# Performance work log

Hardware: AMD Instinct MI355X
Metric: run time of the kernel (lower is better)

Reference implementation:

```python
import jax, jax.numpy as jnp
import numpy as np

NUM_CHANNELS = 512
B_DIM = 64
C_DIM = 16
N = 512
FEAT = NUM_CHANNELS * 4 * 4  # 8192


def setup_inputs() -> dict:
    key = jax.random.key(0)
    k1, k2 = jax.random.split(key)
    inp = jax.random.normal(k1, (N, NUM_CHANNELS, 4, 4), dtype=jnp.float32)
    T = jax.random.normal(k2, (FEAT, B_DIM * C_DIM), dtype=jnp.float32) * 0.1
    return {"inp": inp, "T": T}


def reference(inp, T):
    x = inp.reshape(-1, FEAT)                      # (N, 8192)
    M = (x @ T).reshape(-1, B_DIM, C_DIM)          # (N, B, C)
    # pairwise L1 distance over C: (N, N, B)
    dist = jnp.sum(jnp.abs(M[:, None, :, :] - M[None, :, :, :]), axis=-1)
    o = jnp.sum(jnp.exp(-dist), axis=1)            # (N, B)
    return jnp.concatenate((x, o), axis=1)         # (N, 8192 + B)
```

## Files before the change

kernel.cpp:

```cpp
#include <hip/hip_runtime.h>

#define NROWS 512
#define FEAT  8192
#define BDIM  64
#define CDIM  16
#define MCOLS 1024
#define OUTC  8256
#define KSPLIT 8
#define KCHUNK (FEAT / KSPLIT)
#define MSIZE  (NROWS * MCOLS)

typedef __bf16 bf16x8 __attribute__((ext_vector_type(8)));
typedef float  floatx4 __attribute__((ext_vector_type(4)));

#define AS1 __attribute__((address_space(1)))
#define AS3 __attribute__((address_space(3)))

static __device__ __forceinline__ void gload16(const void* g, void* l) {
    __builtin_amdgcn_global_load_lds((AS1 void*)(g), (AS3 void*)(l), 16, 0, 0);
}

static __device__ __forceinline__ unsigned short f2bf(float f) {
    unsigned int x = __builtin_bit_cast(unsigned int, f);
    unsigned int r = (x + 0x7FFFu + ((x >> 16) & 1u)) >> 16;
    return (unsigned short)r;
}

__global__ __launch_bounds__(512, 2) void k_prep(const float* __restrict__ x,
                                                 const float* __restrict__ T,
                                                 unsigned short* __restrict__ xb,
                                                 unsigned short* __restrict__ Tt,
                                                 float* __restrict__ out) {
    __shared__ __align__(16) float lds[2][64][65];
    int bid = blockIdx.x, t = threadIdx.x;
#pragma unroll
    for (int u = 0; u < 8; ++u) {
        int gid = bid * 4096 + u * 512 + t;
        float4 v = *(const float4*)(x + (size_t)gid * 4);
        ushort4 uu;
        uu.x = f2bf(v.x); uu.y = f2bf(v.y); uu.z = f2bf(v.z); uu.w = f2bf(v.w);
        *(ushort4*)(xb + (size_t)gid * 4) = uu;
        int row = gid >> 11, col4 = gid & 2047;
        *(float4*)(out + (size_t)row * OUTC + col4 * 4) = v;
    }
    int sub = t >> 8, tt = t & 255;
    for (int u = 0; u < 4; ++u) {
        int tile = bid * 8 + u * 2 + sub;
        int kt = tile & 127, nt = tile >> 7;
        __syncthreads();
        int kk = tt >> 2, q = tt & 3;
#pragma unroll
        for (int p = 0; p < 4; ++p) {
            int c4 = q + p * 4;
            float4 v = *(const float4*)(T + (size_t)(kt * 64 + kk) * MCOLS + nt * 64 + c4 * 4);
            lds[sub][kk][c4 * 4 + 0] = v.x; lds[sub][kk][c4 * 4 + 1] = v.y;
            lds[sub][kk][c4 * 4 + 2] = v.z; lds[sub][kk][c4 * 4 + 3] = v.w;
        }
        __syncthreads();
        int nr = tt >> 2, ck = tt & 3;
        unsigned int wv[8];
#pragma unroll
        for (int j = 0; j < 8; ++j) {
            unsigned int lo = f2bf(lds[sub][ck * 16 + j * 2 + 0][nr]);
            unsigned int hi = f2bf(lds[sub][ck * 16 + j * 2 + 1][nr]);
            wv[j] = lo | (hi << 16);
        }
        uint4* dst = (uint4*)(Tt + (size_t)(nt * 64 + nr) * FEAT + kt * 64 + ck * 16);
        dst[0] = make_uint4(wv[0], wv[1], wv[2], wv[3]);
        dst[1] = make_uint4(wv[4], wv[5], wv[6], wv[7]);
    }
}

__global__ __launch_bounds__(256, 2) void k_gemm(const unsigned short* __restrict__ xb,
                                                 const unsigned short* __restrict__ Tt,
                                                 float* __restrict__ Mp) {
    __shared__ __align__(16) unsigned short ldsA[128 * 64];
    __shared__ __align__(16) unsigned short ldsB[64 * 64];
    int bid = blockIdx.x, t = threadIdx.x;
    int mt = bid & 3, nt = (bid >> 2) & 15, ks = bid >> 6;
    int m0 = mt * 128, n0 = nt * 64, kbase = ks * KCHUNK;
    int w = t >> 6, l = t & 63;

    int c  = (l & 3) ^ ((l >> 3) & 3);
    int lr = l >> 2;
    const unsigned short* gA0 = xb + (size_t)(m0 + w * 32 + lr) * FEAT + kbase + c * 8;
    const unsigned short* gA1 = gA0 + (size_t)16 * FEAT;
    const unsigned short* gB0 = Tt + (size_t)(n0 + w * 16 + lr) * FEAT + kbase + c * 8;
    unsigned short* lA00 = ldsA + (4 * w + 0) * 512;
    unsigned short* lA01 = ldsA + (4 * w + 1) * 512;
    unsigned short* lA10 = ldsA + (4 * w + 2) * 512;
    unsigned short* lA11 = ldsA + (4 * w + 3) * 512;
    unsigned short* lB0  = ldsB + (2 * w + 0) * 512;
    unsigned short* lB1  = ldsB + (2 * w + 1) * 512;

    int wr = w >> 1, wc = w & 1, fm = l & 15, fq = l >> 4;
    int fo = fm * 32 + ((fq ^ ((fm >> 1) & 3)) * 8);
    const unsigned short* paB = ldsA + (wr * 8) * 512 + fo;
    const unsigned short* pbB = ldsB + (wc * 4) * 512 + fo;

    floatx4 acc[4][2] = {};

    for (int kk = 0; kk < KCHUNK; kk += 64) {
        __syncthreads();
        gload16(gA0 + kk,      lA00);
        gload16(gA0 + kk + 32, lA01);
        gload16(gA1 + kk,      lA10);
        gload16(gA1 + kk + 32, lA11);
        gload16(gB0 + kk,      lB0);
        gload16(gB0 + kk + 32, lB1);
        __syncthreads();
#pragma unroll
        for (int h = 0; h < 2; ++h) {
            bf16x8 af[4], bfr[2];
#pragma unroll
            for (int a = 0; a < 4; ++a) af[a]  = *(const bf16x8*)(paB + (a * 2 + h) * 512);
#pragma unroll
            for (int b = 0; b < 2; ++b) bfr[b] = *(const bf16x8*)(pbB + (b * 2 + h) * 512);
#pragma unroll
            for (int a = 0; a < 4; ++a)
#pragma unroll
                for (int b = 0; b < 2; ++b)
                    acc[a][b] = __builtin_amdgcn_mfma_f32_16x16x32_bf16(af[a], bfr[b], acc[a][b], 0, 0, 0);
        }
    }

    float* outp = Mp + (size_t)ks * MSIZE;
    int gr0 = m0 + wr * 64, gc0 = n0 + wc * 32;
#pragma unroll
    for (int a = 0; a < 4; ++a)
#pragma unroll
        for (int r = 0; r < 4; ++r) {
            int row = gr0 + a * 16 + fq * 4 + r;
#pragma unroll
            for (int b = 0; b < 2; ++b)
                outp[(size_t)row * MCOLS + gc0 + b * 16 + fm] = acc[a][b][r];
        }
}

__global__ __launch_bounds__(512, 2) void k_pair(const float* __restrict__ Mp,
                                                 float* __restrict__ out) {
    __shared__ float ldsM[NROWS * 20];
    __shared__ float partial[8][64];
    int bid = blockIdx.x, t = threadIdx.x;
    int b = bid & 63, itp = bid >> 6;
#pragma unroll
    for (int p = 0; p < 4; ++p) {
        int idx = t + p * 512;
        int j = idx >> 2, c4 = idx & 3;
        const float* base = Mp + (size_t)j * MCOLS + b * CDIM + c4 * 4;
        float4 s = *(const float4*)base;
#pragma unroll
        for (int k = 1; k < KSPLIT; ++k) {
            float4 v = *(const float4*)(base + (size_t)k * MSIZE);
            s.x += v.x; s.y += v.y; s.z += v.z; s.w += v.w;
        }
        *(float4*)&ldsM[j * 20 + c4 * 4] = s;
    }
    __syncthreads();

    int lane = t & 63, w = t >> 6, g = t >> 8, wg = (t >> 6) & 3;
    int i = (itp * 2 + g) * 64 + lane;
    float mi[CDIM];
#pragma unroll
    for (int cc = 0; cc < CDIM; ++cc) mi[cc] = ldsM[i * 20 + cc];

    float acc = 0.0f;
    for (int jj = wg * 128; jj < wg * 128 + 128; ++jj) {
        float d = 0.0f;
#pragma unroll
        for (int cc = 0; cc < CDIM; ++cc) d += fabsf(mi[cc] - ldsM[jj * 20 + cc]);
        acc += __expf(-d);
    }
    partial[w][lane] = acc;
    __syncthreads();
    if ((t & 255) < 64) {
        int ii = (itp * 2 + g) * 64 + (t & 63);
        float o = partial[g * 4 + 0][t & 63] + partial[g * 4 + 1][t & 63] +
                  partial[g * 4 + 2][t & 63] + partial[g * 4 + 3][t & 63];
        out[(size_t)ii * OUTC + FEAT + b] = o;
    }
}

extern "C" void kernel_launch(void* const* d_in, const int* in_sizes, int n_in,
                              void* d_out, int out_size, void* d_ws, size_t ws_size,
                              hipStream_t stream) {
    const float* x = (const float*)d_in[0];
    const float* T = (const float*)d_in[1];
    float* out = (float*)d_out;

    unsigned short* xb = (unsigned short*)d_ws;
    unsigned short* Tt = (unsigned short*)((char*)d_ws + (8u << 20));
    float*          Mp = (float*)((char*)d_ws + (24u << 20));

    k_prep<<<256, 512, 0, stream>>>(x, T, xb, Tt, out);
    k_gemm<<<512, 256, 0, stream>>>(xb, Tt, Mp);
    k_pair<<<256, 512, 0, stream>>>(Mp, out);
}
```

Before: 137.3 us.

## Fuse bf16 conversion into GEMM and move x copy into pair kernel

Removes the separate prep kernel. The GEMM now reads fp32 x and T directly, converts them to bf16 in registers and writes them into swizzled LDS tiles, prefetching the next k-step's global loads while the MFMAs run. Tiles grow to 128x128 with 512 threads, and block IDs are remapped. The copy of x into the output now happens inside the pair kernel. This saves a launch and the bf16 round trip through workspace, at the cost of heavier register use and conversion work in the GEMM's inner loop.

```diff
diff --git a/kernel.cpp b/kernel.cpp
--- a/kernel.cpp
+++ b/kernel.cpp
@@ -8,120 +8,103 @@
 #define OUTC  8256
 #define KSPLIT 8
 #define KCHUNK (FEAT / KSPLIT)
+#define KSTEPS (KCHUNK / 64)
 #define MSIZE  (NROWS * MCOLS)
 
 typedef __bf16 bf16x8 __attribute__((ext_vector_type(8)));
 typedef float  floatx4 __attribute__((ext_vector_type(4)));
 
-#define AS1 __attribute__((address_space(1)))
-#define AS3 __attribute__((address_space(3)))
-
-static __device__ __forceinline__ void gload16(const void* g, void* l) {
-    __builtin_amdgcn_global_load_lds((AS1 void*)(g), (AS3 void*)(l), 16, 0, 0);
+static __device__ __forceinline__ unsigned int pk2(float a, float b) {
+    unsigned short lo = __builtin_bit_cast(unsigned short, (__bf16)a);
+    unsigned short hi = __builtin_bit_cast(unsigned short, (__bf16)b);
+    return (unsigned int)lo | ((unsigned int)hi << 16);
 }
 
-static __device__ __forceinline__ unsigned short f2bf(float f) {
-    unsigned int x = __builtin_bit_cast(unsigned int, f);
-    unsigned int r = (x + 0x7FFFu + ((x >> 16) & 1u)) >> 16;
-    return (unsigned short)r;
-}
+__global__ __launch_bounds__(512, 2) void k_gemm(const float* __restrict__ x,
+                                                 const float* __restrict__ T,
+                                                 float* __restrict__ Mp) {
+    __shared__ __align__(16) unsigned short ldsA[128 * 64];
+    __shared__ __align__(16) unsigned short ldsB[128 * 64];
+    char* ldsAc = (char*)ldsA;
+    char* ldsBc = (char*)ldsB;
 
-__global__ __launch_bounds__(512, 2) void k_prep(const float* __restrict__ x,
-                                                 const float* __restrict__ T,
-                                                 unsigned short* __restrict__ xb,
-                                                 unsigned short* __restrict__ Tt,
-                                                 float* __restrict__ out) {
-    __shared__ __align__(16) float lds[2][64][65];
-    int bid = blockIdx.x, t = threadIdx.x;
+    int bid = blockIdx.x;
+    int wg = (bid & 7) * 32 + (bid >> 3);
+    int mt = wg & 3, nt = (wg >> 2) & 7, ks = wg >> 5;
+    int m0 = mt * 128, n0 = nt * 128, kbase = ks * KCHUNK;
+    int t = threadIdx.x, w = t >> 6, l = t & 63;
+
+    int arow = t >> 4, aq = t & 15;
+    const float* gA = x + (size_t)(m0 + arow) * FEAT + kbase + aq * 4;
+    int swa = (arow & 7) ^ ((arow >> 2) & 7);
+    int wA = arow * 128 + (((aq >> 1) ^ swa) << 4) + ((aq & 1) << 3);
+
+    int n4 = t & 31, kg = t >> 5;
+    const float* gB = T + (size_t)(kbase + kg * 4) * MCOLS + n0 + n4 * 4;
+    int wB[4];
 #pragma unroll
-    for (int u = 0; u < 8; ++u) {
-        int gid = bid * 4096 + u * 512 + t;
-        float4 v = *(const float4*)(x + (size_t)gid * 4);
-        ushort4 uu;
-        uu.x = f2bf(v.x); uu.y = f2bf(v.y); uu.z = f2bf(v.z); uu.w = f2bf(v.w);
-        *(ushort4*)(xb + (size_t)gid * 4) = uu;
-        int row = gid >> 11, col4 = gid & 2047;
-        *(float4*)(out + (size_t)row * OUTC + col4 * 4) = v;
+    for (int j = 0; j < 4; ++j) {
+        int n = n4 * 4 + j;
+        int swn = (n & 7) ^ ((n >> 2) & 7);
+        wB[j] = n * 128 + (((kg >> 1) ^ swn) << 4) + ((kg & 1) << 3);
     }
-    int sub = t >> 8, tt = t & 255;
-    for (int u = 0; u < 4; ++u) {
-        int tile = bid * 8 + u * 2 + sub;
-        int kt = tile & 127, nt = tile >> 7;
-        __syncthreads();
-        int kk = tt >> 2, q = tt & 3;
+
+    int wr = w >> 2, wc = w & 3, fm = l & 15, fq = l >> 4;
+    int swf = (fm & 7) ^ ((fm >> 2) & 7);
+    int baseA = (wr * 64 + fm) * 128 + ((fq ^ swf) << 4);
+    int baseB = (wc * 32 + fm) * 128 + ((fq ^ swf) << 4);
+
+    float4 va[4], vb[4];
+    auto issue = [&](int KK) {
+        int kko = KK * 64;
+        va[0] = *(const float4*)(gA + kko);
+        va[1] = *(const float4*)(gA + 32 * FEAT + kko);
+        va[2] = *(const float4*)(gA + 64 * FEAT + kko);
+        va[3] = *(const float4*)(gA + 96 * FEAT + kko);
+        vb[0] = *(const float4*)(gB + (size_t)(kko + 0) * MCOLS);
+        vb[1] = *(const float4*)(gB + (size_t)(kko + 1) * MCOLS);
+        vb[2] = *(const float4*)(gB + (size_t)(kko + 2) * MCOLS);
+        vb[3] = *(const float4*)(gB + (size_t)(kko + 3) * MCOLS);
+    };
+
+    issue(0);
+    floatx4 acc[4][2] = {};
+
+    for (int kk = 0; kk < KSTEPS; ++kk) {
 #pragma unroll
-        for (int p = 0; p < 4; ++p) {
-            int c4 = q + p * 4;
-            float4 v = *(const float4*)(T + (size_t)(kt * 64 + kk) * MCOLS + nt * 64 + c4 * 4);
-            lds[sub][kk][c4 * 4 + 0] = v.x; lds[sub][kk][c4 * 4 + 1] = v.y;
-            lds[sub][kk][c4 * 4 + 2] = v.z; lds[sub][kk][c4 * 4 + 3] = v.w;
+        for (int r = 0; r < 4; ++r) {
+            uint2 u; u.x = pk2(va[r].x, va[r].y); u.y = pk2(va[r].z, va[r].w);
+            *(uint2*)(ldsAc + wA + r * 4096) = u;
+        }
+        {
+            uint2 u;
+            u.x = pk2(vb[0].x, vb[1].x); u.y = pk2(vb[2].x, vb[3].x);
+            *(uint2*)(ldsBc + wB[0]) = u;
+            u.x = pk2(vb[0].y, vb[1].y); u.y = pk2(vb[2].y, vb[3].y);
+            *(uint2*)(ldsBc + wB[1]) = u;
+            u.x = pk2(vb[0].z, vb[1].z); u.y = pk2(vb[2].z, vb[3].z);
+            *(uint2*)(ldsBc + wB[2]) = u;
+            u.x = pk2(vb[0].w, vb[1].w); u.y = pk2(vb[2].w, vb[3].w);
+            *(uint2*)(ldsBc + wB[3]) = u;
         }
         __syncthreads();
-        int nr = tt >> 2, ck = tt & 3;
-        unsigned int wv[8];
-#pragma unroll
-        for (int j = 0; j < 8; ++j) {
-            unsigned int lo = f2bf(lds[sub][ck * 16 + j * 2 + 0][nr]);
-            unsigned int hi = f2bf(lds[sub][ck * 16 + j * 2 + 1][nr]);
-            wv[j] = lo | (hi << 16);
-        }
-        uint4* dst = (uint4*)(Tt + (size_t)(nt * 64 + nr) * FEAT + kt * 64 + ck * 16);
-        dst[0] = make_uint4(wv[0], wv[1], wv[2], wv[3]);
-        dst[1] = make_uint4(wv[4], wv[5], wv[6], wv[7]);
-    }
-}
-
-__global__ __launch_bounds__(256, 2) void k_gemm(const unsigned short* __restrict__ xb,
-                                                 const unsigned short* __restrict__ Tt,
-                                                 float* __restrict__ Mp) {
-    __shared__ __align__(16) unsigned short ldsA[128 * 64];
-    __shared__ __align__(16) unsigned short ldsB[64 * 64];
-    int bid = blockIdx.x, t = threadIdx.x;
-    int mt = bid & 3, nt = (bid >> 2) & 15, ks = bid >> 6;
-    int m0 = mt * 128, n0 = nt * 64, kbase = ks * KCHUNK;
-    int w = t >> 6, l = t & 63;
-
-    int c  = (l & 3) ^ ((l >> 3) & 3);
-    int lr = l >> 2;
-    const unsigned short* gA0 = xb + (size_t)(m0 + w * 32 + lr) * FEAT + kbase + c * 8;
-    const unsigned short* gA1 = gA0 + (size_t)16 * FEAT;
-    const unsigned short* gB0 = Tt + (size_t)(n0 + w * 16 + lr) * FEAT + kbase + c * 8;
-    unsigned short* lA00 = ldsA + (4 * w + 0) * 512;
-    unsigned short* lA01 = ldsA + (4 * w + 1) * 512;
-    unsigned short* lA10 = ldsA + (4 * w + 2) * 512;
-    unsigned short* lA11 = ldsA + (4 * w + 3) * 512;
-    unsigned short* lB0  = ldsB + (2 * w + 0) * 512;
-    unsigned short* lB1  = ldsB + (2 * w + 1) * 512;
-
-    int wr = w >> 1, wc = w & 1, fm = l & 15, fq = l >> 4;
-    int fo = fm * 32 + ((fq ^ ((fm >> 1) & 3)) * 8);
-    const unsigned short* paB = ldsA + (wr * 8) * 512 + fo;
-    const unsigned short* pbB = ldsB + (wc * 4) * 512 + fo;
-
-    floatx4 acc[4][2] = {};
-
-    for (int kk = 0; kk < KCHUNK; kk += 64) {
-        __syncthreads();
-        gload16(gA0 + kk,      lA00);
-        gload16(gA0 + kk + 32, lA01);
-        gload16(gA1 + kk,      lA10);
-        gload16(gA1 + kk + 32, lA11);
-        gload16(gB0 + kk,      lB0);
-        gload16(gB0 + kk + 32, lB1);
-        __syncthreads();
+        if (kk + 1 < KSTEPS) issue(kk + 1);
 #pragma unroll
         for (int h = 0; h < 2; ++h) {
             bf16x8 af[4], bfr[2];
 #pragma unroll
-            for (int a = 0; a < 4; ++a) af[a]  = *(const bf16x8*)(paB + (a * 2 + h) * 512);
+            for (int a = 0; a < 4; ++a)
+                af[a] = *(const bf16x8*)(ldsAc + ((baseA + a * 2048) ^ ((h ^ (a & 1)) << 6)));
 #pragma unroll
-            for (int b = 0; b < 2; ++b) bfr[b] = *(const bf16x8*)(pbB + (b * 2 + h) * 512);
+            for (int b = 0; b < 2; ++b)
+                bfr[b] = *(const bf16x8*)(ldsBc + ((baseB + b * 2048) ^ ((h ^ (b & 1)) << 6)));
 #pragma unroll
             for (int a = 0; a < 4; ++a)
 #pragma unroll
                 for (int b = 0; b < 2; ++b)
                     acc[a][b] = __builtin_amdgcn_mfma_f32_16x16x32_bf16(af[a], bfr[b], acc[a][b], 0, 0, 0);
         }
+        __syncthreads();
     }
 
     float* outp = Mp + (size_t)ks * MSIZE;
@@ -137,12 +120,24 @@
         }
 }
 
-__global__ __launch_bounds__(512, 2) void k_pair(const float* __restrict__ Mp,
+__global__ __launch_bounds__(512, 2) void k_pair(const float* __restrict__ x,
+                                                 const float* __restrict__ Mp,
                                                  float* __restrict__ out) {
     __shared__ float ldsM[NROWS * 20];
     __shared__ float partial[8][64];
     int bid = blockIdx.x, t = threadIdx.x;
     int b = bid & 63, itp = bid >> 6;
+
+    float4 cv[8];
+    {
+        const float* src = x + (size_t)bid * 2 * FEAT;
+#pragma unroll
+        for (int i = 0; i < 8; ++i) {
+            int idx = t + i * 512;
+            cv[i] = *(const float4*)(src + (size_t)(idx >> 11) * FEAT + (idx & 2047) * 4);
+        }
+    }
+
 #pragma unroll
     for (int p = 0; p < 4; ++p) {
         int idx = t + p * 512;
@@ -179,6 +174,15 @@
                   partial[g * 4 + 2][t & 63] + partial[g * 4 + 3][t & 63];
         out[(size_t)ii * OUTC + FEAT + b] = o;
     }
+
+    {
+        float* dst = out + (size_t)bid * 2 * OUTC;
+#pragma unroll
+        for (int i2 = 0; i2 < 8; ++i2) {
+            int idx = t + i2 * 512;
+            *(float4*)(dst + (size_t)(idx >> 11) * OUTC + (idx & 2047) * 4) = cv[i2];
+        }
+    }
 }
 
 extern "C" void kernel_launch(void* const* d_in, const int* in_sizes, int n_in,
@@ -188,11 +192,8 @@
     const float* T = (const float*)d_in[1];
     float* out = (float*)d_out;
 
-    unsigned short* xb = (unsigned short*)d_ws;
-    unsigned short* Tt = (unsigned short*)((char*)d_ws + (8u << 20));
-    float*          Mp = (float*)((char*)d_ws + (24u << 20));
+    float* Mp = (float*)d_ws;
 
-    k_prep<<<256, 512, 0, stream>>>(x, T, xb, Tt, out);
-    k_gemm<<<512, 256, 0, stream>>>(xb, Tt, Mp);
-    k_pair<<<256, 512, 0, stream>>>(Mp, out);
+    k_gemm<<<256, 512, 0, stream>>>(x, T, Mp);
+    k_pair<<<256, 512, 0, stream>>>(x, Mp, out);
 }
```

Measured after the change: 145.3 us. +5.8%, slower.
